# Kernel tuning notes

Hardware: AMD Instinct MI355X
Metric: run time of the kernel (lower is better)

Reference implementation:

```python
import jax, jax.numpy as jnp
import numpy as np
from jax import lax

K = 5  # pn_size (propagation neighborhood)

def _one_hot_kernel(dtype):
    # [k*k, 1, k, k]: channel c has a single 1 at spatial position (c//k, c%k)
    return jnp.eye(K * K, dtype=dtype).reshape(K * K, 1, K, K)

def setup_inputs() -> dict:
    key = jax.random.key(0)
    k1, k2, k3 = jax.random.split(key, 3)
    B, H, W = 8, 512, 512
    return {
        "input_thick": jax.random.uniform(k1, (B, 1, H, W), dtype=jnp.float32),
        "input_thin": jax.random.uniform(k2, (B, 1, H, W), dtype=jnp.float32),
        "agg_coeff": jax.random.uniform(k3, (B, K * K, H, W), dtype=jnp.float32),
    }

def reference(input_thick, input_thin, agg_coeff):
    # elementwise max of the two confidence maps: [B,1,H,W]
    input_sal = jnp.maximum(input_thick, input_thin)
    w = _one_hot_kernel(input_sal.dtype)
    pad = K // 2
    # one-hot conv == unfold: map_sal[b,c,h,w] = input_sal[b,0,h+dh-pad,w+dw-pad]
    map_sal = lax.conv_general_dilated(
        input_sal, w,
        window_strides=(1, 1),
        padding=[(pad, pad), (pad, pad)],
        dimension_numbers=("NCHW", "OIHW", "NCHW"),
    )  # [B, k*k, H, W]
    # weighted channel-sum aggregation -> [B,1,H,W]
    prod_sal = jnp.sum(map_sal * agg_coeff, axis=1, keepdims=True)
    return prod_sal
```

## Files before the change

kernel.cpp:

```cpp
#include <hip/hip_runtime.h>


constexpr int K = 5;
constexpr int PAD = 2;

typedef float vfloat4 __attribute__((ext_vector_type(4)));

__global__ __launch_bounds__(256) void adaptive_agg_kernel(
    const float* __restrict__ thick,
    const float* __restrict__ thin,
    const float* __restrict__ agg,
    float* __restrict__ out,
    int B, int H, int W)
{
    const int wq = W >> 3;
    int tid = blockIdx.x * blockDim.x + threadIdx.x;
    int w0 = (tid % wq) << 3;
    int h  = (tid / wq) % H;
    int b  = tid / (wq * H);
    if (b >= B) return;

    const size_t plane = (size_t)H * W;
    const float* tk  = thick + (size_t)b * plane;
    const float* tn  = thin  + (size_t)b * plane;
    const float* ag0 = agg + (size_t)b * (K * K) * plane + (size_t)h * W + w0;

    float acc[8];
    #pragma unroll
    for (int p = 0; p < 8; ++p) acc[p] = 0.f;

    const int a0 = (w0 >= 4) ? (w0 - 4) : 0;
    const int a3 = (w0 + 8 <= W - 4) ? (w0 + 8) : (W - 4);

    #pragma unroll
    for (int dh = 0; dh < K; ++dh) {
        int hh = h + dh - PAD;
        if (hh < 0 || hh >= H) continue;
        const float* tkr = tk + (size_t)hh * W;
        const float* tnr = tn + (size_t)hh * W;

        vfloat4 t0 = *(const vfloat4*)(tkr + a0);
        vfloat4 t1 = *(const vfloat4*)(tkr + w0);
        vfloat4 t2 = *(const vfloat4*)(tkr + w0 + 4);
        vfloat4 t3 = *(const vfloat4*)(tkr + a3);
        vfloat4 n0 = *(const vfloat4*)(tnr + a0);
        vfloat4 n1 = *(const vfloat4*)(tnr + w0);
        vfloat4 n2 = *(const vfloat4*)(tnr + w0 + 4);
        vfloat4 n3 = *(const vfloat4*)(tnr + a3);

        float srow[16];
        #pragma unroll
        for (int e = 0; e < 4; ++e) {
            srow[0 + e]  = fmaxf(t0[e], n0[e]);
            srow[4 + e]  = fmaxf(t1[e], n1[e]);
            srow[8 + e]  = fmaxf(t2[e], n2[e]);
            srow[12 + e] = fmaxf(t3[e], n3[e]);
        }
        #pragma unroll
        for (int j = 0; j < 16; ++j) {
            int ww = w0 - 4 + j;
            srow[j] = (ww >= 0 && ww < W) ? srow[j] : 0.f;
        }

        const float* ag = ag0 + (size_t)(dh * K) * plane;
        #pragma unroll
        for (int dw = 0; dw < K; ++dw) {
            const float* ap = ag + (size_t)dw * plane;
            vfloat4 c0 = __builtin_nontemporal_load((const vfloat4*)ap);
            vfloat4 c1 = __builtin_nontemporal_load((const vfloat4*)(ap + 4));
            #pragma unroll
            for (int e = 0; e < 4; ++e) {
                acc[e]     = fmaf(c0[e], srow[2 + dw + e],     acc[e]);
                acc[4 + e] = fmaf(c1[e], srow[2 + dw + 4 + e], acc[4 + e]);
            }
        }
    }

    float* op = out + (size_t)b * plane + (size_t)h * W + w0;
    vfloat4 o0 = { acc[0], acc[1], acc[2], acc[3] };
    vfloat4 o1 = { acc[4], acc[5], acc[6], acc[7] };
    __builtin_nontemporal_store(o0, (vfloat4*)op);
    __builtin_nontemporal_store(o1, (vfloat4*)(op + 4));
}

extern "C" void kernel_launch(void* const* d_in, const int* in_sizes, int n_in,
                              void* d_out, int out_size, void* d_ws, size_t ws_size,
                              hipStream_t stream) {
    const float* thick = (const float*)d_in[0];
    const float* thin  = (const float*)d_in[1];
    const float* agg   = (const float*)d_in[2];
    float* out = (float*)d_out;

    const int H = 512, W = 512;
    const int B = in_sizes[0] / (H * W);

    int total = B * H * (W / 8);
    int block = 256;
    int grid = (total + block - 1) / block;
    adaptive_agg_kernel<<<grid, block, 0, stream>>>(thick, thin, agg, out, B, H, W);
}
```

Before: 293.0 us.

## Precompute zero-padded saliency map in workspace, then aggregate without bounds checks

Splits the work into two kernels. The first computes max(thick, thin) into a zero-padded workspace buffer. The second reads the padded map with no boundary masking and uses scalar (readfirstlane) base offsets with 32-bit indexing. This removes the per-tap double loads, the fmax and the border selects from the main kernel. In exchange it adds an extra kernel launch and a write-then-read of a padded saliency plane through global memory.

```diff
diff --git a/kernel.cpp b/kernel.cpp
--- a/kernel.cpp
+++ b/kernel.cpp
@@ -2,72 +2,77 @@
 
 
 constexpr int K = 5;
-constexpr int PAD = 2;
+constexpr int HH = 512, WW = 512;
+constexpr int SW = WW + 16;
+constexpr int SH = HH + 4;
+constexpr int SPLANE = SH * SW;
+constexpr int PLANE = HH * WW;
 
-typedef float vfloat4 __attribute__((ext_vector_type(4)));
+typedef float vf4 __attribute__((ext_vector_type(4)));
 
-__global__ __launch_bounds__(256) void adaptive_agg_kernel(
+__global__ __launch_bounds__(256) void sal_pad_kernel(
     const float* __restrict__ thick,
     const float* __restrict__ thin,
+    float* __restrict__ sal, int B)
+{
+    const int nw = SW / 4;
+    int tid = blockIdx.x * blockDim.x + threadIdx.x;
+    int wp = (tid % nw) * 4;
+    int hp = (tid / nw) % SH;
+    int b  = tid / (nw * SH);
+    if (b >= B) return;
+
+    vf4 v = {0.f, 0.f, 0.f, 0.f};
+    int h = hp - 2, w = wp - 8;
+    if (h >= 0 && h < HH && w >= 0 && w < WW) {
+        const float* tk = thick + ((size_t)b * HH + h) * WW + w;
+        const float* tn = thin  + ((size_t)b * HH + h) * WW + w;
+        vf4 a = *(const vf4*)tk;
+        vf4 c = *(const vf4*)tn;
+        v.x = fmaxf(a.x, c.x); v.y = fmaxf(a.y, c.y);
+        v.z = fmaxf(a.z, c.z); v.w = fmaxf(a.w, c.w);
+    }
+    *(vf4*)(sal + (size_t)b * SPLANE + (size_t)hp * SW + wp) = v;
+}
+
+__global__ __launch_bounds__(256) void agg_kernel(
+    const float* __restrict__ sal,
     const float* __restrict__ agg,
-    float* __restrict__ out,
-    int B, int H, int W)
+    float* __restrict__ out, int B)
 {
-    const int wq = W >> 3;
+    const int wq = WW >> 3;
     int tid = blockIdx.x * blockDim.x + threadIdx.x;
     int w0 = (tid % wq) << 3;
-    int h  = (tid / wq) % H;
-    int b  = tid / (wq * H);
+    int h  = (tid / wq) % HH;
+    int b  = tid / (wq * HH);
     if (b >= B) return;
 
-    const size_t plane = (size_t)H * W;
-    const float* tk  = thick + (size_t)b * plane;
-    const float* tn  = thin  + (size_t)b * plane;
-    const float* ag0 = agg + (size_t)b * (K * K) * plane + (size_t)h * W + w0;
+    int sal_base = __builtin_amdgcn_readfirstlane(b * SPLANE + h * SW + 8);
+    int agg_base = __builtin_amdgcn_readfirstlane(b * (K * K) * PLANE + h * WW);
+    int out_base = __builtin_amdgcn_readfirstlane(b * PLANE + h * WW);
 
     float acc[8];
     #pragma unroll
     for (int p = 0; p < 8; ++p) acc[p] = 0.f;
 
-    const int a0 = (w0 >= 4) ? (w0 - 4) : 0;
-    const int a3 = (w0 + 8 <= W - 4) ? (w0 + 8) : (W - 4);
-
     #pragma unroll
     for (int dh = 0; dh < K; ++dh) {
-        int hh = h + dh - PAD;
-        if (hh < 0 || hh >= H) continue;
-        const float* tkr = tk + (size_t)hh * W;
-        const float* tnr = tn + (size_t)hh * W;
-
-        vfloat4 t0 = *(const vfloat4*)(tkr + a0);
-        vfloat4 t1 = *(const vfloat4*)(tkr + w0);
-        vfloat4 t2 = *(const vfloat4*)(tkr + w0 + 4);
-        vfloat4 t3 = *(const vfloat4*)(tkr + a3);
-        vfloat4 n0 = *(const vfloat4*)(tnr + a0);
-        vfloat4 n1 = *(const vfloat4*)(tnr + w0);
-        vfloat4 n2 = *(const vfloat4*)(tnr + w0 + 4);
-        vfloat4 n3 = *(const vfloat4*)(tnr + a3);
-
+        const float* srp = sal + sal_base + dh * SW + (w0 - 4);
+        vf4 s0 = *(const vf4*)(srp);
+        vf4 s1 = *(const vf4*)(srp + 4);
+        vf4 s2 = *(const vf4*)(srp + 8);
+        vf4 s3 = *(const vf4*)(srp + 12);
         float srow[16];
         #pragma unroll
         for (int e = 0; e < 4; ++e) {
-            srow[0 + e]  = fmaxf(t0[e], n0[e]);
-            srow[4 + e]  = fmaxf(t1[e], n1[e]);
-            srow[8 + e]  = fmaxf(t2[e], n2[e]);
-            srow[12 + e] = fmaxf(t3[e], n3[e]);
+            srow[e] = s0[e]; srow[4 + e] = s1[e];
+            srow[8 + e] = s2[e]; srow[12 + e] = s3[e];
         }
         #pragma unroll
-        for (int j = 0; j < 16; ++j) {
-            int ww = w0 - 4 + j;
-            srow[j] = (ww >= 0 && ww < W) ? srow[j] : 0.f;
-        }
-
-        const float* ag = ag0 + (size_t)(dh * K) * plane;
-        #pragma unroll
         for (int dw = 0; dw < K; ++dw) {
-            const float* ap = ag + (size_t)dw * plane;
-            vfloat4 c0 = __builtin_nontemporal_load((const vfloat4*)ap);
-            vfloat4 c1 = __builtin_nontemporal_load((const vfloat4*)(ap + 4));
+            const float* ap = agg + agg_base + (dh * K + dw) * PLANE + w0;
+            vf4 c0 = __builtin_nontemporal_load((const vf4*)ap);
+            vf4 c1 = __builtin_nontemporal_load((const vf4*)(ap + 4));
             #pragma unroll
             for (int e = 0; e < 4; ++e) {
                 acc[e]     = fmaf(c0[e], srow[2 + dw + e],     acc[e]);
@@ -76,11 +81,11 @@
         }
     }
 
-    float* op = out + (size_t)b * plane + (size_t)h * W + w0;
-    vfloat4 o0 = { acc[0], acc[1], acc[2], acc[3] };
-    vfloat4 o1 = { acc[4], acc[5], acc[6], acc[7] };
-    __builtin_nontemporal_store(o0, (vfloat4*)op);
-    __builtin_nontemporal_store(o1, (vfloat4*)(op + 4));
+    float* op = out + out_base + w0;
+    vf4 o0 = {acc[0], acc[1], acc[2], acc[3]};
+    vf4 o1 = {acc[4], acc[5], acc[6], acc[7]};
+    __builtin_nontemporal_store(o0, (vf4*)op);
+    __builtin_nontemporal_store(o1, (vf4*)(op + 4));
 }
 
 extern "C" void kernel_launch(void* const* d_in, const int* in_sizes, int n_in,
@@ -90,12 +95,13 @@
     const float* thin  = (const float*)d_in[1];
     const float* agg   = (const float*)d_in[2];
     float* out = (float*)d_out;
+    float* sal = (float*)d_ws;
 
-    const int H = 512, W = 512;
-    const int B = in_sizes[0] / (H * W);
+    const int B = in_sizes[0] / PLANE;
 
-    int total = B * H * (W / 8);
-    int block = 256;
-    int grid = (total + block - 1) / block;
-    adaptive_agg_kernel<<<grid, block, 0, stream>>>(thick, thin, agg, out, B, H, W);
+    int t1 = B * SH * (SW / 4);
+    sal_pad_kernel<<<(t1 + 255) / 256, 256, 0, stream>>>(thick, thin, sal, B);
+
+    int t2 = B * HH * (WW / 8);
+    agg_kernel<<<(t2 + 255) / 256, 256, 0, stream>>>(sal, agg, out, B);
 }
```

Result: slower. 307.9 us (+5.1%).
